# Performance work log

Measured on AMD Instinct MI355X. Metric: run time of the kernel, lower is better.

The kernel has to match this reference:

```python
import jax, jax.numpy as jnp
import numpy as np

B, L, D = 2, 4096, 1024
H = 8
DK = D // H          # 128 head qk dim (expand_k=1)
DV = 2 * D // H      # 256 head v dim (expand_v=2)
FFN = 4 * D          # 4096
CHUNK = 64
EPS = 1e-6


def _ln(x, w, b):
    mu = x.mean(-1, keepdims=True)
    var = ((x - mu) ** 2).mean(-1, keepdims=True)
    return (x - mu) / jnp.sqrt(var + EPS) * w + b


def _retention(q, k, v):
    # q,k: [B,H,L,DK], v: [B,H,L,DV]; RetNet decayed causal linear attention,
    # computed chunkwise (intra-chunk parallel + inter-chunk recurrent state).
    Bq, Hq, Lq, Dk = q.shape
    Dv = v.shape[-1]
    N = Lq // CHUNK
    b = 1.0 - jnp.exp2(-5.0 - jnp.arange(Hq, dtype=q.dtype))   # [H] per-head decay
    logb = jnp.log(b)
    q = q * (Dk ** -0.5)
    t = jnp.arange(CHUNK, dtype=q.dtype)
    diff = t[:, None] - t[None, :]                              # [C,C]
    mask = jnp.where(diff >= 0, jnp.exp(logb[:, None, None] * diff), 0.0)  # [H,C,C]
    d_q = jnp.exp(logb[:, None] * (t[None, :] + 1.0))           # b^(t+1), [H,C]
    d_k = jnp.exp(logb[:, None] * (CHUNK - 1.0 - t[None, :]))   # b^(C-1-s), [H,C]
    d_c = jnp.exp(logb * CHUNK)                                 # b^C, [H]

    def to_chunks(x):
        return x.reshape(Bq, Hq, N, CHUNK, -1).transpose(2, 0, 1, 3, 4)  # [N,B,H,C,d]

    qc, kc, vc = to_chunks(q), to_chunks(k), to_chunks(v)
    S0 = jnp.zeros((Bq, Hq, Dk, Dv), q.dtype)

    def step(S, inp):
        qi, ki, vi = inp                                        # [B,H,C,*]
        A = jnp.einsum('bhtd,bhsd->bhts', qi, ki) * mask        # intra-chunk scores
        o = jnp.einsum('bhts,bhsv->bhtv', A, vi)
        o = o + jnp.einsum('bhtd,bhdv->bhtv', qi * d_q[None, :, :, None], S)
        S = S * d_c[None, :, None, None] + jnp.einsum('bhsd,bhsv->bhdv', ki * d_k[None, :, :, None], vi)
        return S, o

    _, os = jax.lax.scan(step, S0, (qc, kc, vc))                # os: [N,B,H,C,DV]
    return os.transpose(1, 2, 0, 3, 4).reshape(Bq, Hq, Lq, Dv)


def setup_inputs() -> dict:
    key = jax.random.key(0)
    ks = jax.random.split(key, 8)
    s = 0.02
    return {
        'x': jax.random.normal(ks[0], (B, L, D), jnp.float32),
        'ln1_w': jnp.ones((D,), jnp.float32),
        'ln1_b': jnp.zeros((D,), jnp.float32),
        'Wq': jax.random.normal(ks[1], (D, D), jnp.float32) * s,
        'Wk': jax.random.normal(ks[2], (D, D), jnp.float32) * s,
        'Wv': jax.random.normal(ks[3], (D, 2 * D), jnp.float32) * s,
        'Wo': jax.random.normal(ks[4], (2 * D, D), jnp.float32) * s,
        'ln2_w': jnp.ones((D,), jnp.float32),
        'ln2_b': jnp.zeros((D,), jnp.float32),
        'W1': jax.random.normal(ks[5], (D, FFN), jnp.float32) * s,
        'b1': jnp.zeros((FFN,), jnp.float32),
        'W2': jax.random.normal(ks[6], (FFN, D), jnp.float32) * s,
        'b2': jnp.zeros((D,), jnp.float32),
    }


def reference(x, ln1_w, ln1_b, Wq, Wk, Wv, Wo, ln2_w, ln2_b, W1, b1, W2, b2):
    # retention branch
    h = _ln(x, ln1_w, ln1_b)
    q = (h @ Wq).reshape(B, L, H, DK).transpose(0, 2, 1, 3)
    k = (h @ Wk).reshape(B, L, H, DK).transpose(0, 2, 1, 3)
    v = (h @ Wv).reshape(B, L, H, DV).transpose(0, 2, 1, 3)
    o = _retention(q, k, v)                                      # [B,H,L,DV]
    o = o.transpose(0, 2, 1, 3).reshape(B, L, H * DV)
    x = x + o @ Wo
    # FFN branch (exact gelu, no subln, eval-mode dropout)
    f = _ln(x, ln2_w, ln2_b)
    f = jax.nn.gelu(f @ W1 + b1, approximate=False)
    x = x + (f @ W2 + b2)
    return x
```

## Files before the change

### kernel.cpp

```cpp
#include <hip/hip_runtime.h>
#include <math.h>

typedef short s16;
typedef __attribute__((ext_vector_type(8))) short short8;
typedef __attribute__((ext_vector_type(4))) float f32x4;

__device__ __forceinline__ float bf2f_lo(unsigned u){ return __builtin_bit_cast(float, u << 16); }
__device__ __forceinline__ float bf2f_hi(unsigned u){ return __builtin_bit_cast(float, u & 0xffff0000u); }
__device__ __forceinline__ float bf2f(unsigned short h){ return __builtin_bit_cast(float, (unsigned)h << 16); }
__device__ __forceinline__ s16 f2bf(float f){
  unsigned u = __builtin_bit_cast(unsigned, f);
  u += 0x7fffu + ((u >> 16) & 1u);
  return (s16)(u >> 16);
}
__device__ __forceinline__ void unpack8(int4 v, float* f){
  unsigned a=(unsigned)v.x, b=(unsigned)v.y, c=(unsigned)v.z, d=(unsigned)v.w;
  f[0]=bf2f_lo(a); f[1]=bf2f_hi(a); f[2]=bf2f_lo(b); f[3]=bf2f_hi(b);
  f[4]=bf2f_lo(c); f[5]=bf2f_hi(c); f[6]=bf2f_lo(d); f[7]=bf2f_hi(d);
}
__device__ __forceinline__ void gl2lds16(const s16* g, s16* l){
  __builtin_amdgcn_global_load_lds((const __attribute__((address_space(1))) void*)g,
                                   (__attribute__((address_space(3))) void*)l, 16, 0, 0);
}

__global__ __launch_bounds__(256) void ln_bf16(const float* __restrict__ x,
                                               const float* __restrict__ w,
                                               const float* __restrict__ b,
                                               s16* __restrict__ out){
  int row = blockIdx.x; int t = threadIdx.x;
  const float* xr = x + (size_t)row * 1024;
  float4 v = *(const float4*)(xr + t*4);
  float s = v.x + v.y + v.z + v.w;
  float ss = v.x*v.x + v.y*v.y + v.z*v.z + v.w*v.w;
  for (int o = 32; o > 0; o >>= 1){ s += __shfl_down(s, o, 64); ss += __shfl_down(ss, o, 64); }
  __shared__ float red[8];
  int wid = t >> 6, lane = t & 63;
  if (lane == 0){ red[wid] = s; red[4+wid] = ss; }
  __syncthreads();
  if (t == 0){
    float S = red[0]+red[1]+red[2]+red[3];
    float SS = red[4]+red[5]+red[6]+red[7];
    red[0] = S * (1.f/1024.f);
    red[1] = SS * (1.f/1024.f);
  }
  __syncthreads();
  float mu = red[0];
  float var = red[1] - mu*mu;
  float rstd = rsqrtf(var + 1e-6f);
  float vv[4] = {v.x, v.y, v.z, v.w};
  short4 o4;
  s16 tmp[4];
  #pragma unroll
  for (int i = 0; i < 4; ++i){
    int c = t*4 + i;
    float val = (vv[i] - mu) * rstd * w[c] + b[c];
    tmp[i] = f2bf(val);
  }
  o4.x = tmp[0]; o4.y = tmp[1]; o4.z = tmp[2]; o4.w = tmp[3];
  *(short4*)(out + (size_t)row*1024 + t*4) = o4;
}

__global__ __launch_bounds__(256) void conv_t(const float* __restrict__ W,
                                              s16* __restrict__ Wt,
                                              int K, int N, float scale){
  __shared__ float tile[32][33];
  int n0 = blockIdx.x * 32, k0 = blockIdx.y * 32;
  int tx = threadIdx.x & 31, ty = threadIdx.x >> 5;
  #pragma unroll
  for (int i = 0; i < 4; ++i){
    int r = ty + i*8;
    tile[r][tx] = W[(size_t)(k0 + r)*N + n0 + tx];
  }
  __syncthreads();
  #pragma unroll
  for (int i = 0; i < 4; ++i){
    int r = ty + i*8;
    Wt[(size_t)(n0 + r)*K + k0 + tx] = f2bf(tile[tx][r] * scale);
  }
}

__global__ __launch_bounds__(256,2) void gemm_nt(const s16* __restrict__ A,
                                                 const s16* __restrict__ Bt,
                                                 int M, int N, int K, int ldb,
                                                 float* __restrict__ Cf,
                                                 s16* __restrict__ Cb,
                                                 const float* __restrict__ bias,
                                                 const float* __restrict__ resid,
                                                 int flags){
  __shared__ s16 As[128*32];
  __shared__ s16 Bs[128*32];
  int t = threadIdx.x;
  int m0 = blockIdx.y * 128, n0 = blockIdx.x * 128;
  int w = t >> 6, lane = t & 63;
  int wm = (w >> 1) * 64, wn = (w & 1) * 64;
  int lrow = lane & 15, lq = lane >> 4;
  f32x4 acc[4][4];
  #pragma unroll
  for (int i = 0; i < 4; ++i)
    #pragma unroll
    for (int j = 0; j < 4; ++j) acc[i][j] = (f32x4){0.f,0.f,0.f,0.f};

  const s16* Ag = A  + (size_t)(m0 + (t>>2)) * K   + (t&3)*8;
  const s16* Bg = Bt + (size_t)(n0 + (t>>2)) * ldb + (t&3)*8;
  s16* lA0 = As + w*512;
  s16* lA1 = As + 2048 + w*512;
  s16* lB0 = Bs + w*512;
  s16* lB1 = Bs + 2048 + w*512;

  for (int k0 = 0; k0 < K; k0 += 32){
    __syncthreads();
    gl2lds16(Ag + k0, lA0);
    gl2lds16(Ag + (size_t)64*K + k0, lA1);
    gl2lds16(Bg + k0, lB0);
    gl2lds16(Bg + (size_t)64*ldb + k0, lB1);
    __syncthreads();
    short8 af[4], bfr[4];
    #pragma unroll
    for (int mi = 0; mi < 4; ++mi)
      af[mi] = *(short8*)&As[(wm + mi*16 + lrow)*32 + lq*8];
    #pragma unroll
    for (int ni = 0; ni < 4; ++ni)
      bfr[ni] = *(short8*)&Bs[(wn + ni*16 + lrow)*32 + lq*8];
    #pragma unroll
    for (int mi = 0; mi < 4; ++mi)
      #pragma unroll
      for (int ni = 0; ni < 4; ++ni)
        acc[mi][ni] = __builtin_amdgcn_mfma_f32_16x16x32_bf16(af[mi], bfr[ni], acc[mi][ni], 0, 0, 0);
  }

  bool do_gelu = flags & 1;
  bool out_bf = flags & 2;
  #pragma unroll
  for (int mi = 0; mi < 4; ++mi){
    #pragma unroll
    for (int ni = 0; ni < 4; ++ni){
      int gcol = n0 + wn + ni*16 + lrow;
      float bcol = bias ? bias[gcol] : 0.f;
      int grow_base = m0 + wm + mi*16 + lq*4;
      #pragma unroll
      for (int r = 0; r < 4; ++r){
        int grow = grow_base + r;
        float val = acc[mi][ni][r] + bcol;
        if (do_gelu) val = 0.5f * val * (1.f + erff(val * 0.70710678118654752f));
        if (resid) val += resid[(size_t)grow * N + gcol];
        if (out_bf) Cb[(size_t)grow * N + gcol] = f2bf(val);
        else        Cf[(size_t)grow * N + gcol] = val;
      }
    }
  }
}

__global__ __launch_bounds__(256,2) void ret_chunksum(const s16* __restrict__ k,
                                                      const s16* __restrict__ v,
                                                      s16* __restrict__ U){
  int bi = blockIdx.x;
  int h = bi & 7, n = bi >> 3;
  int t = threadIdx.x;
  __shared__ s16 ks[128*72];
  __shared__ s16 vs[256*72];
  float log2b = log2f(1.f - exp2f(-5.f - (float)h));
  const s16* kbase = k + (size_t)(n*64)*1024 + h*128;
  const s16* vbase = v + (size_t)(n*64)*2048 + h*256;
  #pragma unroll
  for (int i = 0; i < 4; ++i){
    int e = i*2048 + t*8;
    int s = e >> 7, dk = e & 127;
    int4 kv = *(const int4*)(kbase + (size_t)s*1024 + dk);
    float f[8]; unpack8(kv, f);
    float dec = exp2f(log2b * (float)(63 - s));
    #pragma unroll
    for (int j = 0; j < 8; ++j) ks[(dk+j)*72 + s] = f2bf(f[j]*dec);
  }
  #pragma unroll
  for (int i = 0; i < 8; ++i){
    int e = i*2048 + t*8;
    int s = e >> 8, dv = e & 255;
    int4 vv = *(const int4*)(vbase + (size_t)s*2048 + dv);
    s16 tmp[8]; *(int4*)tmp = vv;
    #pragma unroll
    for (int j = 0; j < 8; ++j) vs[(dv+j)*72 + s] = tmp[j];
  }
  __syncthreads();
  int w = t >> 6, lane = t & 63;
  int m0w = w*64;
  int lrow = lane & 15, lq = lane >> 4;
  f32x4 acc[4][8];
  #pragma unroll
  for (int mi = 0; mi < 4; ++mi)
    #pragma unroll
    for (int ni = 0; ni < 8; ++ni) acc[mi][ni] = (f32x4){0.f,0.f,0.f,0.f};
  #pragma unroll
  for (int kk = 0; kk < 64; kk += 32){
    short8 af[4], bfr[8];
    #pragma unroll
    for (int mi = 0; mi < 4; ++mi)
      af[mi] = *(short8*)&vs[(m0w + mi*16 + lrow)*72 + kk + lq*8];
    #pragma unroll
    for (int ni = 0; ni < 8; ++ni)
      bfr[ni] = *(short8*)&ks[(ni*16 + lrow)*72 + kk + lq*8];
    #pragma unroll
    for (int mi = 0; mi < 4; ++mi)
      #pragma unroll
      for (int ni = 0; ni < 8; ++ni)
        acc[mi][ni] = __builtin_amdgcn_mfma_f32_16x16x32_bf16(af[mi], bfr[ni], acc[mi][ni], 0, 0, 0);
  }
  s16* Ub = U + ((size_t)(h*64 + n))*32768;
  #pragma unroll
  for (int mi = 0; mi < 4; ++mi)
    #pragma unroll
    for (int ni = 0; ni < 8; ++ni)
      #pragma unroll
      for (int r = 0; r < 4; ++r){
        int row = m0w + mi*16 + lq*4 + r;
        int col = ni*16 + lrow;
        Ub[(size_t)row*128 + col] = f2bf(acc[mi][ni][r]);
      }
}

__global__ __launch_bounds__(256) void ret_scan(s16* __restrict__ US){
  int tid = blockIdx.x*256 + threadIdx.x;
  int h = tid >> 12;
  int rem = tid & 4095;
  int dv = rem >> 4, dk0 = (rem & 15)*8;
  float log2b = log2f(1.f - exp2f(-5.f - (float)h));
  float dc = exp2f(log2b * 64.f);
  s16* base = US + (size_t)h*64*32768 + (size_t)dv*128 + dk0;
  float acc[8] = {0.f,0.f,0.f,0.f,0.f,0.f,0.f,0.f};
  #pragma unroll 4
  for (int n = 0; n < 64; ++n){
    s16* p = base + (size_t)n*32768;
    int4 u4 = *(const int4*)p;
    float uf[8]; unpack8(u4, uf);
    s16 sb[8];
    #pragma unroll
    for (int j = 0; j < 8; ++j) sb[j] = f2bf(acc[j]);
    *(int4*)p = *(int4*)sb;
    #pragma unroll
    for (int j = 0; j < 8; ++j) acc[j] = acc[j]*dc + uf[j];
  }
}

__global__ __launch_bounds__(256,2) void ret_attn(const s16* __restrict__ q,
                                                  const s16* __restrict__ k,
                                                  const s16* __restrict__ v,
                                                  const s16* __restrict__ S,
                                                  s16* __restrict__ o){
  int bi = blockIdx.x;
  int h = bi & 7, n = bi >> 3;
  int t = threadIdx.x;
  int w = t >> 6, lane = t & 63;
  int lrow = lane & 15, lq = lane >> 4;
  float log2b = log2f(1.f - exp2f(-5.f - (float)h));
  __shared__ s16 As[64*72];
  __shared__ s16 vs[256*72];

  const s16* vbase = v + (size_t)(n*64)*2048 + h*256;
  #pragma unroll
  for (int i = 0; i < 8; ++i){
    int e = i*2048 + t*8;
    int s = e >> 8, dv = e & 255;
    int4 vv = *(const int4*)(vbase + (size_t)s*2048 + dv);
    s16 tmp[8]; *(int4*)tmp = vv;
    #pragma unroll
    for (int j = 0; j < 8; ++j) vs[(dv+j)*72 + s] = tmp[j];
  }

  const s16* qbase = q + (size_t)(n*64)*1024 + h*128;
  const s16* kbase = k + (size_t)(n*64)*1024 + h*128;
  short8 qf[4][4];
  #pragma unroll
  for (int ti = 0; ti < 4; ++ti)
    #pragma unroll
    for (int c = 0; c < 4; ++c)
      qf[ti][c] = *(const short8*)(qbase + (size_t)(ti*16 + lrow)*1024 + c*32 + lq*8);
  short8 kf[4];
  #pragma unroll
  for (int c = 0; c < 4; ++c)
    kf[c] = *(const short8*)(kbase + (size_t)(16*w + lrow)*1024 + c*32 + lq*8);
  #pragma unroll
  for (int ti = 0; ti < 4; ++ti){
    f32x4 acc_a = (f32x4){0.f,0.f,0.f,0.f};
    #pragma unroll
    for (int c = 0; c < 4; ++c)
      acc_a = __builtin_amdgcn_mfma_f32_16x16x32_bf16(qf[ti][c], kf[c], acc_a, 0, 0, 0);
    #pragma unroll
    for (int r = 0; r < 4; ++r){
      int ti_idx = ti*16 + lq*4 + r;
      int s_idx = 16*w + lrow;
      int d = ti_idx - s_idx;
      float val = (d >= 0) ? acc_a[r] * exp2f(log2b * (float)d) : 0.f;
      As[ti_idx*72 + s_idx] = f2bf(val);
    }
  }
  __syncthreads();

  f32x4 acc[4][4];
  #pragma unroll
  for (int mi = 0; mi < 4; ++mi)
    #pragma unroll
    for (int nj = 0; nj < 4; ++nj) acc[mi][nj] = (f32x4){0.f,0.f,0.f,0.f};

  const s16* Sbase = S + ((size_t)(h*64 + n)*256 + w*64)*128;
  #pragma unroll
  for (int c = 0; c < 4; ++c){
    short8 bf[4];
    #pragma unroll
    for (int nj = 0; nj < 4; ++nj)
      bf[nj] = *(const short8*)(Sbase + (size_t)(nj*16 + lrow)*128 + c*32 + lq*8);
    #pragma unroll
    for (int mi = 0; mi < 4; ++mi)
      #pragma unroll
      for (int nj = 0; nj < 4; ++nj)
        acc[mi][nj] = __builtin_amdgcn_mfma_f32_16x16x32_bf16(qf[mi][c], bf[nj], acc[mi][nj], 0, 0, 0);
  }
  #pragma unroll
  for (int mi = 0; mi < 4; ++mi){
    #pragma unroll
    for (int r = 0; r < 4; ++r){
      float dq = exp2f(log2b * (float)(mi*16 + lq*4 + r + 1));
      #pragma unroll
      for (int nj = 0; nj < 4; ++nj) acc[mi][nj][r] *= dq;
    }
  }
  #pragma unroll
  for (int c = 0; c < 2; ++c){
    short8 af[4], bf[4];
    #pragma unroll
    for (int mi = 0; mi < 4; ++mi)
      af[mi] = *(short8*)&As[(mi*16 + lrow)*72 + c*32 + lq*8];
    #pragma unroll
    for (int nj = 0; nj < 4; ++nj)
      bf[nj] = *(short8*)&vs[(w*64 + nj*16 + lrow)*72 + c*32 + lq*8];
    #pragma unroll
    for (int mi = 0; mi < 4; ++mi)
      #pragma unroll
      for (int nj = 0; nj < 4; ++nj)
        acc[mi][nj] = __builtin_amdgcn_mfma_f32_16x16x32_bf16(af[mi], bf[nj], acc[mi][nj], 0, 0, 0);
  }
  s16* obase = o + (size_t)(n*64)*2048 + h*256;
  #pragma unroll
  for (int mi = 0; mi < 4; ++mi)
    #pragma unroll
    for (int nj = 0; nj < 4; ++nj)
      #pragma unroll
      for (int r = 0; r < 4; ++r){
        int row = mi*16 + lq*4 + r;
        int col = w*64 + nj*16 + lrow;
        obase[(size_t)row*2048 + col] = f2bf(acc[mi][nj][r]);
      }
}

extern "C" void kernel_launch(void* const* d_in, const int* in_sizes, int n_in,
                              void* d_out, int out_size, void* d_ws, size_t ws_size,
                              hipStream_t stream) {
  (void)in_sizes; (void)n_in; (void)out_size; (void)ws_size;
  const float* x     = (const float*)d_in[0];
  const float* ln1_w = (const float*)d_in[1];
  const float* ln1_b = (const float*)d_in[2];
  const float* Wq    = (const float*)d_in[3];
  const float* Wk    = (const float*)d_in[4];
  const float* Wv    = (const float*)d_in[5];
  const float* Wo    = (const float*)d_in[6];
  const float* ln2_w = (const float*)d_in[7];
  const float* ln2_b = (const float*)d_in[8];
  const float* W1    = (const float*)d_in[9];
  const float* b1    = (const float*)d_in[10];
  const float* W2    = (const float*)d_in[11];
  const float* b2    = (const float*)d_in[12];
  float* out = (float*)d_out;
  char* ws = (char*)d_ws;

  const size_t MB = 1ull << 20;
  s16* Wq_t = (s16*)(ws + 0*MB);
  s16* Wk_t = (s16*)(ws + 2*MB);
  s16* Wv_t = (s16*)(ws + 4*MB);
  s16* Wo_t = (s16*)(ws + 8*MB);
  s16* W1_t = (s16*)(ws + 12*MB);
  s16* W2_t = (s16*)(ws + 20*MB);
  s16* hbuf = (s16*)(ws + 28*MB);
  s16* h2   = (s16*)(ws + 28*MB);
  s16* qb   = (s16*)(ws + 44*MB);
  s16* kb   = (s16*)(ws + 60*MB);
  s16* vb   = (s16*)(ws + 76*MB);
  float* x1 = (float*)(ws + 44*MB);
  s16* fb   = (s16*)(ws + 76*MB);
  s16* US   = (s16*)(ws + 108*MB);
  s16* ob   = (s16*)(ws + 140*MB);

  conv_t<<<dim3(32,32),  256, 0, stream>>>(Wq, Wq_t, 1024, 1024, 0.08838834764831845f);
  conv_t<<<dim3(32,32),  256, 0, stream>>>(Wk, Wk_t, 1024, 1024, 1.f);
  conv_t<<<dim3(64,32),  256, 0, stream>>>(Wv, Wv_t, 1024, 2048, 1.f);
  conv_t<<<dim3(32,64),  256, 0, stream>>>(Wo, Wo_t, 2048, 1024, 1.f);
  conv_t<<<dim3(128,32), 256, 0, stream>>>(W1, W1_t, 1024, 4096, 1.f);
  conv_t<<<dim3(32,128), 256, 0, stream>>>(W2, W2_t, 4096, 1024, 1.f);

  ln_bf16<<<8192, 256, 0, stream>>>(x, ln1_w, ln1_b, hbuf);

  gemm_nt<<<dim3(8,64),  256, 0, stream>>>(hbuf, Wq_t, 8192, 1024, 1024, 1024, nullptr, qb, nullptr, nullptr, 2);
  gemm_nt<<<dim3(8,64),  256, 0, stream>>>(hbuf, Wk_t, 8192, 1024, 1024, 1024, nullptr, kb, nullptr, nullptr, 2);
  gemm_nt<<<dim3(16,64), 256, 0, stream>>>(hbuf, Wv_t, 8192, 2048, 1024, 1024, nullptr, vb, nullptr, nullptr, 2);

  for (int b = 0; b < 2; ++b){
    const s16* qb_b = qb + (size_t)b*4096*1024;
    const s16* kb_b = kb + (size_t)b*4096*1024;
    const s16* vb_b = vb + (size_t)b*4096*2048;
    s16* ob_b = ob + (size_t)b*4096*2048;
    ret_chunksum<<<512, 256, 0, stream>>>(kb_b, vb_b, US);
    ret_scan<<<128, 256, 0, stream>>>(US);
    ret_attn<<<512, 256, 0, stream>>>(qb_b, kb_b, vb_b, US, ob_b);
  }

  gemm_nt<<<dim3(8,64),  256, 0, stream>>>(ob, Wo_t, 8192, 1024, 2048, 2048, x1, nullptr, nullptr, x, 0);
  ln_bf16<<<8192, 256, 0, stream>>>(x1, ln2_w, ln2_b, h2);

  gemm_nt<<<dim3(16,64), 256, 0, stream>>>(h2, W1_t, 8192, 2048, 1024, 1024, nullptr, fb, b1, nullptr, 2|1);
  gemm_nt<<<dim3(8,64),  256, 0, stream>>>(fb, W2_t, 8192, 1024, 2048, 4096, out, nullptr, b2, x1, 0);
  gemm_nt<<<dim3(16,64), 256, 0, stream>>>(h2, W1_t + (size_t)2048*1024, 8192, 2048, 1024, 1024, nullptr, fb, b1 + 2048, nullptr, 2|1);
  gemm_nt<<<dim3(8,64),  256, 0, stream>>>(fb, W2_t + 2048, 8192, 1024, 2048, 4096, out, nullptr, nullptr, out, 0);
}
```

Measured before the change: 720.0 us.

## Fuse QKV projections and FFN halves, add 64x128-tile GEMM for N=1024

Concatenates the transposed Wq/Wk/Wv into one weight buffer so a single GEMM writes an interleaved [L, 4096] qkv tensor. The retention kernels now read q, k and v with a 4096 row stride. The two-pass FFN split is merged into one W1 GEMM (N=4096) and one W2 GEMM (K=4096), which removes the extra launches and the output read-modify-write. A new gemm_nt_h kernel with a 64x128 tile and no LDS double buffering doubles the block count for the N=1024 output GEMMs (Wo, W2) to fill the GPU better, at the cost of less data reuse per block.

```diff
diff --git a/kernel.cpp b/kernel.cpp
--- a/kernel.cpp
+++ b/kernel.cpp
@@ -150,6 +150,74 @@
   }
 }
 
+__global__ __launch_bounds__(256,2) void gemm_nt_h(const s16* __restrict__ A,
+                                                   const s16* __restrict__ Bt,
+                                                   int M, int N, int K, int ldb,
+                                                   float* __restrict__ Cf,
+                                                   s16* __restrict__ Cb,
+                                                   const float* __restrict__ bias,
+                                                   const float* __restrict__ resid,
+                                                   int flags){
+  __shared__ s16 As[64*32];
+  __shared__ s16 Bs[128*32];
+  int t = threadIdx.x;
+  int m0 = blockIdx.y * 64, n0 = blockIdx.x * 128;
+  int w = t >> 6, lane = t & 63;
+  int lrow = lane & 15, lq = lane >> 4;
+  f32x4 acc[4][2];
+  #pragma unroll
+  for (int i = 0; i < 4; ++i)
+    #pragma unroll
+    for (int j = 0; j < 2; ++j) acc[i][j] = (f32x4){0.f,0.f,0.f,0.f};
+
+  const s16* Ag = A  + (size_t)(m0 + (t>>2)) * K   + (t&3)*8;
+  const s16* Bg = Bt + (size_t)(n0 + (t>>2)) * ldb + (t&3)*8;
+  s16* lA  = As + w*512;
+  s16* lB0 = Bs + w*512;
+  s16* lB1 = Bs + 2048 + w*512;
+
+  for (int k0 = 0; k0 < K; k0 += 32){
+    __syncthreads();
+    gl2lds16(Ag + k0, lA);
+    gl2lds16(Bg + k0, lB0);
+    gl2lds16(Bg + (size_t)64*ldb + k0, lB1);
+    __syncthreads();
+    short8 af[4], bfr[2];
+    #pragma unroll
+    for (int mi = 0; mi < 4; ++mi)
+      af[mi] = *(short8*)&As[(mi*16 + lrow)*32 + lq*8];
+    #pragma unroll
+    for (int ni = 0; ni < 2; ++ni)
+      bfr[ni] = *(short8*)&Bs[(w*32 + ni*16 + lrow)*32 + lq*8];
+    #pragma unroll
+    for (int mi = 0; mi < 4; ++mi)
+      #pragma unroll
+      for (int ni = 0; ni < 2; ++ni)
+        acc[mi][ni] = __builtin_amdgcn_mfma_f32_16x16x32_bf16(af[mi], bfr[ni], acc[mi][ni], 0, 0, 0);
+  }
+
+  bool do_gelu = flags & 1;
+  bool out_bf = flags & 2;
+  #pragma unroll
+  for (int mi = 0; mi < 4; ++mi){
+    #pragma unroll
+    for (int ni = 0; ni < 2; ++ni){
+      int gcol = n0 + w*32 + ni*16 + lrow;
+      float bcol = bias ? bias[gcol] : 0.f;
+      int grow_base = m0 + mi*16 + lq*4;
+      #pragma unroll
+      for (int r = 0; r < 4; ++r){
+        int grow = grow_base + r;
+        float val = acc[mi][ni][r] + bcol;
+        if (do_gelu) val = 0.5f * val * (1.f + erff(val * 0.70710678118654752f));
+        if (resid) val += resid[(size_t)grow * N + gcol];
+        if (out_bf) Cb[(size_t)grow * N + gcol] = f2bf(val);
+        else        Cf[(size_t)grow * N + gcol] = val;
+      }
+    }
+  }
+}
+
 __global__ __launch_bounds__(256,2) void ret_chunksum(const s16* __restrict__ k,
                                                       const s16* __restrict__ v,
                                                       s16* __restrict__ U){
@@ -159,13 +227,13 @@
   __shared__ s16 ks[128*72];
   __shared__ s16 vs[256*72];
   float log2b = log2f(1.f - exp2f(-5.f - (float)h));
-  const s16* kbase = k + (size_t)(n*64)*1024 + h*128;
-  const s16* vbase = v + (size_t)(n*64)*2048 + h*256;
+  const s16* kbase = k + (size_t)(n*64)*4096 + h*128;
+  const s16* vbase = v + (size_t)(n*64)*4096 + h*256;
   #pragma unroll
   for (int i = 0; i < 4; ++i){
     int e = i*2048 + t*8;
     int s = e >> 7, dk = e & 127;
-    int4 kv = *(const int4*)(kbase + (size_t)s*1024 + dk);
+    int4 kv = *(const int4*)(kbase + (size_t)s*4096 + dk);
     float f[8]; unpack8(kv, f);
     float dec = exp2f(log2b * (float)(63 - s));
     #pragma unroll
@@ -175,7 +243,7 @@
   for (int i = 0; i < 8; ++i){
     int e = i*2048 + t*8;
     int s = e >> 8, dv = e & 255;
-    int4 vv = *(const int4*)(vbase + (size_t)s*2048 + dv);
+    int4 vv = *(const int4*)(vbase + (size_t)s*4096 + dv);
     s16 tmp[8]; *(int4*)tmp = vv;
     #pragma unroll
     for (int j = 0; j < 8; ++j) vs[(dv+j)*72 + s] = tmp[j];
@@ -254,29 +322,29 @@
   __shared__ s16 As[64*72];
   __shared__ s16 vs[256*72];
 
-  const s16* vbase = v + (size_t)(n*64)*2048 + h*256;
+  const s16* vbase = v + (size_t)(n*64)*4096 + h*256;
   #pragma unroll
   for (int i = 0; i < 8; ++i){
     int e = i*2048 + t*8;
     int s = e >> 8, dv = e & 255;
-    int4 vv = *(const int4*)(vbase + (size_t)s*2048 + dv);
+    int4 vv = *(const int4*)(vbase + (size_t)s*4096 + dv);
     s16 tmp[8]; *(int4*)tmp = vv;
     #pragma unroll
     for (int j = 0; j < 8; ++j) vs[(dv+j)*72 + s] = tmp[j];
   }
 
-  const s16* qbase = q + (size_t)(n*64)*1024 + h*128;
-  const s16* kbase = k + (size_t)(n*64)*1024 + h*128;
+  const s16* qbase = q + (size_t)(n*64)*4096 + h*128;
+  const s16* kbase = k + (size_t)(n*64)*4096 + h*128;
   short8 qf[4][4];
   #pragma unroll
   for (int ti = 0; ti < 4; ++ti)
     #pragma unroll
     for (int c = 0; c < 4; ++c)
-      qf[ti][c] = *(const short8*)(qbase + (size_t)(ti*16 + lrow)*1024 + c*32 + lq*8);
+      qf[ti][c] = *(const short8*)(qbase + (size_t)(ti*16 + lrow)*4096 + c*32 + lq*8);
   short8 kf[4];
   #pragma unroll
   for (int c = 0; c < 4; ++c)
-    kf[c] = *(const short8*)(kbase + (size_t)(16*w + lrow)*1024 + c*32 + lq*8);
+    kf[c] = *(const short8*)(kbase + (size_t)(16*w + lrow)*4096 + c*32 + lq*8);
   #pragma unroll
   for (int ti = 0; ti < 4; ++ti){
     f32x4 acc_a = (f32x4){0.f,0.f,0.f,0.f};
@@ -371,50 +439,42 @@
   char* ws = (char*)d_ws;
 
   const size_t MB = 1ull << 20;
-  s16* Wq_t = (s16*)(ws + 0*MB);
-  s16* Wk_t = (s16*)(ws + 2*MB);
-  s16* Wv_t = (s16*)(ws + 4*MB);
+  s16* Wqkv_t = (s16*)(ws + 0*MB);
   s16* Wo_t = (s16*)(ws + 8*MB);
   s16* W1_t = (s16*)(ws + 12*MB);
   s16* W2_t = (s16*)(ws + 20*MB);
   s16* hbuf = (s16*)(ws + 28*MB);
   s16* h2   = (s16*)(ws + 28*MB);
-  s16* qb   = (s16*)(ws + 44*MB);
-  s16* kb   = (s16*)(ws + 60*MB);
-  s16* vb   = (s16*)(ws + 76*MB);
+  s16* qkv  = (s16*)(ws + 44*MB);
   float* x1 = (float*)(ws + 44*MB);
   s16* fb   = (s16*)(ws + 76*MB);
   s16* US   = (s16*)(ws + 108*MB);
   s16* ob   = (s16*)(ws + 140*MB);
 
-  conv_t<<<dim3(32,32),  256, 0, stream>>>(Wq, Wq_t, 1024, 1024, 0.08838834764831845f);
-  conv_t<<<dim3(32,32),  256, 0, stream>>>(Wk, Wk_t, 1024, 1024, 1.f);
-  conv_t<<<dim3(64,32),  256, 0, stream>>>(Wv, Wv_t, 1024, 2048, 1.f);
+  conv_t<<<dim3(32,32),  256, 0, stream>>>(Wq, Wqkv_t, 1024, 1024, 0.08838834764831845f);
+  conv_t<<<dim3(32,32),  256, 0, stream>>>(Wk, Wqkv_t + (size_t)1024*1024, 1024, 1024, 1.f);
+  conv_t<<<dim3(64,32),  256, 0, stream>>>(Wv, Wqkv_t + (size_t)2048*1024, 1024, 2048, 1.f);
   conv_t<<<dim3(32,64),  256, 0, stream>>>(Wo, Wo_t, 2048, 1024, 1.f);
   conv_t<<<dim3(128,32), 256, 0, stream>>>(W1, W1_t, 1024, 4096, 1.f);
   conv_t<<<dim3(32,128), 256, 0, stream>>>(W2, W2_t, 4096, 1024, 1.f);
 
   ln_bf16<<<8192, 256, 0, stream>>>(x, ln1_w, ln1_b, hbuf);
 
-  gemm_nt<<<dim3(8,64),  256, 0, stream>>>(hbuf, Wq_t, 8192, 1024, 1024, 1024, nullptr, qb, nullptr, nullptr, 2);
-  gemm_nt<<<dim3(8,64),  256, 0, stream>>>(hbuf, Wk_t, 8192, 1024, 1024, 1024, nullptr, kb, nullptr, nullptr, 2);
-  gemm_nt<<<dim3(16,64), 256, 0, stream>>>(hbuf, Wv_t, 8192, 2048, 1024, 1024, nullptr, vb, nullptr, nullptr, 2);
+  gemm_nt<<<dim3(32,64), 256, 0, stream>>>(hbuf, Wqkv_t, 8192, 4096, 1024, 1024, nullptr, qkv, nullptr, nullptr, 2);
 
   for (int b = 0; b < 2; ++b){
-    const s16* qb_b = qb + (size_t)b*4096*1024;
-    const s16* kb_b = kb + (size_t)b*4096*1024;
-    const s16* vb_b = vb + (size_t)b*4096*2048;
+    const s16* q_b = qkv + (size_t)b*4096*4096;
+    const s16* k_b = q_b + 1024;
+    const s16* v_b = q_b + 2048;
     s16* ob_b = ob + (size_t)b*4096*2048;
-    ret_chunksum<<<512, 256, 0, stream>>>(kb_b, vb_b, US);
+    ret_chunksum<<<512, 256, 0, stream>>>(k_b, v_b, US);
     ret_scan<<<128, 256, 0, stream>>>(US);
-    ret_attn<<<512, 256, 0, stream>>>(qb_b, kb_b, vb_b, US, ob_b);
-  }
-
-  gemm_nt<<<dim3(8,64),  256, 0, stream>>>(ob, Wo_t, 8192, 1024, 2048, 2048, x1, nullptr, nullptr, x, 0);
+    ret_attn<<<512, 256, 0, stream>>>(q_b, k_b, v_b, US, ob_b);
+  }
+
+  gemm_nt_h<<<dim3(8,128), 256, 0, stream>>>(ob, Wo_t, 8192, 1024, 2048, 2048, x1, nullptr, nullptr, x, 0);
   ln_bf16<<<8192, 256, 0, stream>>>(x1, ln2_w, ln2_b, h2);
 
-  gemm_nt<<<dim3(16,64), 256, 0, stream>>>(h2, W1_t, 8192, 2048, 1024, 1024, nullptr, fb, b1, nullptr, 2|1);
-  gemm_nt<<<dim3(8,64),  256, 0, stream>>>(fb, W2_t, 8192, 1024, 2048, 4096, out, nullptr, b2, x1, 0);
-  gemm_nt<<<dim3(16,64), 256, 0, stream>>>(h2, W1_t + (size_t)2048*1024, 8192, 2048, 1024, 1024, nullptr, fb, b1 + 2048, nullptr, 2|1);
-  gemm_nt<<<dim3(8,64),  256, 0, stream>>>(fb, W2_t + 2048, 8192, 1024, 2048, 4096, out, nullptr, nullptr, out, 0);
-}
+  gemm_nt<<<dim3(32,64), 256, 0, stream>>>(h2, W1_t, 8192, 4096, 1024, 1024, nullptr, fb, b1, nullptr, 2|1);
+  gemm_nt_h<<<dim3(8,128), 256, 0, stream>>>(fb, W2_t, 8192, 1024, 4096, 4096, out, nullptr, b2, x1, 0);
+}
```

After: 680.1 us. 5.5% less time.
